# Kernel optimization log

Hardware: AMD Instinct MI355X
Metric: run time of the kernel (lower is better)

Reference implementation:

```python
import jax, jax.numpy as jnp
import numpy as np

NHEAD = 8


def setup_inputs() -> dict:
    key = jax.random.key(0)
    ks = jax.random.split(key, 11)
    B, N, T, D = 8, 64, 128, 512
    s = 1.0 / np.sqrt(D)
    x = jax.random.normal(ks[0], (B, N, T, D), dtype=jnp.float32)
    mask = jax.random.randint(ks[1], (B, N, T, 1), 0, 2).astype(jnp.float32)
    Wq = jax.random.normal(ks[2], (D, D), dtype=jnp.float32) * s
    bq = jax.random.normal(ks[3], (D,), dtype=jnp.float32) * 0.01
    Wk = jax.random.normal(ks[4], (D, D), dtype=jnp.float32) * s
    bk = jax.random.normal(ks[5], (D,), dtype=jnp.float32) * 0.01
    Wv = jax.random.normal(ks[6], (D, D), dtype=jnp.float32) * s
    bv = jax.random.normal(ks[7], (D,), dtype=jnp.float32) * 0.01
    Wo = jax.random.normal(ks[8], (D, D), dtype=jnp.float32) * s
    bo = jax.random.normal(ks[9], (D,), dtype=jnp.float32) * 0.01
    return {"x": x, "mask": mask, "Wq": Wq, "bq": bq, "Wk": Wk, "bk": bk,
            "Wv": Wv, "bv": bv, "Wo": Wo, "bo": bo}


def _attention(x, mask, Wq, bq, Wk, bk, Wv, bv, Wo, bo):
    B, N, T, D = x.shape
    H = NHEAD
    Dh = D // H
    xf = x.reshape(B * N, T, D)  # fold batch*num_node
    # QKV projections -> [BN, H, T, Dh]
    Q = (xf @ Wq + bq).reshape(B * N, T, H, Dh).transpose(0, 2, 1, 3)
    K = (xf @ Wk + bk).reshape(B * N, T, H, Dh).transpose(0, 2, 1, 3)
    V = (xf @ Wv + bv).reshape(B * N, T, H, Dh).transpose(0, 2, 1, 3)
    # outer-product mask: [BN, 1, T, T], broadcasts over heads
    mf = mask.reshape(B * N, T)
    cmask = (mf[:, :, None] * mf[:, None, :])[:, None, :, :]
    valid = cmask != 0
    scale = 1.0 / jnp.sqrt(jnp.float32(Dh))
    scores = jnp.einsum('bhqd,bhkd->bhqk', Q, K) * scale  # [BN,H,T,T]
    # masked softmax; fully-masked rows become 0 (matches softmax -> nan_to_num)
    s = jnp.where(valid, scores, -1e30)
    m = jnp.max(s, axis=-1, keepdims=True)
    e = jnp.where(valid, jnp.exp(s - m), 0.0)
    denom = jnp.sum(e, axis=-1, keepdims=True)
    attn = jnp.where(denom > 0, e / jnp.where(denom > 0, denom, 1.0), 0.0)
    out = jnp.einsum('bhqk,bhkd->bhqd', attn, V)  # [BN,H,T,Dh]
    out = out.transpose(0, 2, 1, 3).reshape(B * N, T, D)
    out = out @ Wo + bo
    return out.reshape(B, N, T, D)


def reference(x, mask, Wq, bq, Wk, bk, Wv, bv, Wo, bo):
    return _attention(x, mask, Wq, bq, Wk, bk, Wv, bv, Wo, bo)
```

## Files before the change

kernel.cpp:

```cpp
#include <hip/hip_runtime.h>
#include <hip/hip_bf16.h>

#define BN   512
#define TT   128
#define DD   512
#define HH   8
#define DH   64
#define MTOT (BN * TT)

typedef __attribute__((ext_vector_type(8))) _Float16 half8v;
typedef __attribute__((ext_vector_type(4))) float    float4v;

#define AS1 __attribute__((address_space(1)))
#define AS3 __attribute__((address_space(3)))

union Hbits { _Float16 f; ushort u; };

__global__ __launch_bounds__(256)
void cvt_x(const float* __restrict__ X, _Float16* __restrict__ Xh) {
    const size_t total = (size_t)MTOT * DD / 4;
    for (size_t i = (size_t)blockIdx.x * 256 + threadIdx.x; i < total;
         i += (size_t)gridDim.x * 256) {
        float4 v = *(const float4*)(X + i * 4);
        Hbits h0, h1, h2, h3;
        h0.f = (_Float16)v.x; h1.f = (_Float16)v.y;
        h2.f = (_Float16)v.z; h3.f = (_Float16)v.w;
        *(ushort4*)(Xh + i * 4) = make_ushort4(h0.u, h1.u, h2.u, h3.u);
    }
}

__global__ __launch_bounds__(256)
void cvt_w(const float* __restrict__ W, _Float16* __restrict__ Wh) {
    int idx = blockIdx.x * 256 + threadIdx.x;
    int n = idx >> 9;
    int k = idx & 511;
    Wh[(size_t)n * DD + k] = (_Float16)W[(size_t)k * DD + n];
}

template <int MODE>
__global__ __launch_bounds__(256)
void gemm_mfma(const _Float16* __restrict__ A,
               const _Float16* __restrict__ W0,
               const _Float16* __restrict__ W1,
               const _Float16* __restrict__ W2,
               const float* __restrict__ b0, const float* __restrict__ b1,
               const float* __restrict__ b2,
               void* __restrict__ O0, void* __restrict__ O1,
               void* __restrict__ O2) {
    __shared__ _Float16 Alds[128 * 64];
    __shared__ _Float16 Blds[128 * 64];

    const int mt = blockIdx.x, nt = blockIdx.y, wz = blockIdx.z;
    const _Float16* Bt = (wz == 0) ? W0 : (wz == 1) ? W1 : W2;
    const float* bias = (wz == 0) ? b0 : (wz == 1) ? b1 : b2;

    const int tid = threadIdx.x;
    const int lane = tid & 63;
    const int wid = tid >> 6;
    const int wr = wid >> 1, wc = wid & 1;
    const int m0 = mt * 128, n0 = nt * 128;

    float4v acc[4][4] = {};

    for (int kt = 0; kt < 8; ++kt) {
        const int k0 = kt * 64;
        __syncthreads();
#pragma unroll
        for (int r = 0; r < 4; ++r) {
            const int ubase = r * 256 + wid * 64;
            const int u = ubase + lane;
            const int row = u >> 3, c = u & 7;
            const int csrc = c ^ (row & 7);
            const _Float16* gpA = A + (size_t)(m0 + row) * DD + k0 + csrc * 8;
            __builtin_amdgcn_global_load_lds(
                (const AS1 void*)gpA, (AS3 void*)(Alds + ubase * 8), 16, 0, 0);
            const _Float16* gpB = Bt + (size_t)(n0 + row) * DD + k0 + csrc * 8;
            __builtin_amdgcn_global_load_lds(
                (const AS1 void*)gpB, (AS3 void*)(Blds + ubase * 8), 16, 0, 0);
        }
        __syncthreads();

#pragma unroll
        for (int ks = 0; ks < 2; ++ks) {
            const int g = ks * 4 + (lane >> 4);
            const int cswz = (g ^ (lane & 7)) * 8;
            half8v a[4], b[4];
#pragma unroll
            for (int i = 0; i < 4; ++i)
                a[i] = *(const half8v*)(Alds +
                        (size_t)(wr * 64 + i * 16 + (lane & 15)) * 64 + cswz);
#pragma unroll
            for (int j = 0; j < 4; ++j)
                b[j] = *(const half8v*)(Blds +
                        (size_t)(wc * 64 + j * 16 + (lane & 15)) * 64 + cswz);
#pragma unroll
            for (int i = 0; i < 4; ++i)
#pragma unroll
                for (int j = 0; j < 4; ++j)
                    acc[i][j] = __builtin_amdgcn_mfma_f32_16x16x32_f16(
                        a[i], b[j], acc[i][j], 0, 0, 0);
        }
    }

    const int cr = (lane >> 4) * 4;
    const int cc0 = lane & 15;
    if (MODE == 0) {
        float* C = (float*)((wz == 0) ? O0 : (wz == 1) ? O1 : O2);
#pragma unroll
        for (int j = 0; j < 4; ++j) {
            const int col = n0 + wc * 64 + j * 16 + cc0;
            const float bv = bias[col];
#pragma unroll
            for (int i = 0; i < 4; ++i) {
                const size_t rbase = (size_t)(m0 + wr * 64 + i * 16 + cr);
#pragma unroll
                for (int rg = 0; rg < 4; ++rg)
                    C[(rbase + rg) * DD + col] = acc[i][j][rg] + bv;
            }
        }
    } else if (wz < 2) {
        _Float16* C = (_Float16*)((wz == 0) ? O0 : O1);
#pragma unroll
        for (int j = 0; j < 4; ++j) {
            const int col = n0 + wc * 64 + j * 16 + cc0;
            const float bv = bias[col];
#pragma unroll
            for (int i = 0; i < 4; ++i) {
                const size_t rbase = (size_t)(m0 + wr * 64 + i * 16 + cr);
#pragma unroll
                for (int rg = 0; rg < 4; ++rg)
                    C[(rbase + rg) * DD + col] = (_Float16)(acc[i][j][rg] + bv);
            }
        }
    } else {
        _Float16* Vt = (_Float16*)O2;
        const int bnq = m0 >> 7;
#pragma unroll
        for (int j = 0; j < 4; ++j) {
            const int col = n0 + wc * 64 + j * 16 + cc0;
            const int hh = col >> 6, d = col & 63;
            const float bv = bias[col];
#pragma unroll
            for (int i = 0; i < 4; ++i) {
                const int t0 = wr * 64 + i * 16 + cr;
                Hbits e0, e1, e2, e3;
                e0.f = (_Float16)(acc[i][j][0] + bv);
                e1.f = (_Float16)(acc[i][j][1] + bv);
                e2.f = (_Float16)(acc[i][j][2] + bv);
                e3.f = (_Float16)(acc[i][j][3] + bv);
                *(ushort4*)(Vt + ((size_t)(bnq * 8 + hh) * 64 + d) * 128 + t0)
                    = make_ushort4(e0.u, e1.u, e2.u, e3.u);
            }
        }
    }
}

__global__ __launch_bounds__(256)
void attn_mfma(const _Float16* __restrict__ Qh, const _Float16* __restrict__ Kh,
               const _Float16* __restrict__ Vt, const float* __restrict__ mask,
               _Float16* __restrict__ Oh) {
    __shared__ _Float16 KP[128 * 128];
    __shared__ _Float16 Vl[64 * 128];
    __shared__ float maskS[TT];

    const int bnh = blockIdx.x, bn = bnh >> 3, h = bnh & 7;
    const int tid = threadIdx.x, lane = tid & 63, wid = tid >> 6;
    const int l15 = lane & 15, l16 = lane >> 4;

    if (tid < TT) maskS[tid] = mask[bn * TT + tid];

#pragma unroll
    for (int it = 0; it < 4; ++it) {
        const int ubase = it * 256 + wid * 64;
        const int u = ubase + lane;
        const int row = u >> 3, c = u & 7;
        const _Float16* gp = Kh + (size_t)(bn * TT + row) * DD + h * DH +
                             (c ^ (row & 7)) * 8;
        __builtin_amdgcn_global_load_lds(
            (const AS1 void*)gp, (AS3 void*)(KP + ubase * 8), 16, 0, 0);
    }
#pragma unroll
    for (int it = 0; it < 4; ++it) {
        const int ubase = it * 256 + wid * 64;
        const int u = ubase + lane;
        const int row = u >> 4, c = u & 15;
        const _Float16* gp = Vt + ((size_t)(bn * HH + h) * 64 + row) * 128 +
                             (c ^ (row & 15)) * 8;
        __builtin_amdgcn_global_load_lds(
            (const AS1 void*)gp, (AS3 void*)(Vl + ubase * 8), 16, 0, 0);
    }
    half8v qf[2][2];
#pragma unroll
    for (int i = 0; i < 2; ++i)
#pragma unroll
        for (int ks = 0; ks < 2; ++ks)
            qf[i][ks] = *(const half8v*)(Qh +
                (size_t)(bn * TT + wid * 32 + i * 16 + l15) * DD +
                h * DH + ks * 32 + l16 * 8);
    __syncthreads();

    float4v s[2][8] = {};
#pragma unroll
    for (int ks = 0; ks < 2; ++ks) {
#pragma unroll
        for (int j = 0; j < 8; ++j) {
            const int row = j * 16 + l15;
            const int g = ks * 4 + l16;
            half8v bf = *(const half8v*)(KP + (size_t)row * 64 +
                                         ((g ^ (l15 & 7)) * 8));
            s[0][j] = __builtin_amdgcn_mfma_f32_16x16x32_f16(
                qf[0][ks], bf, s[0][j], 0, 0, 0);
            s[1][j] = __builtin_amdgcn_mfma_f32_16x16x32_f16(
                qf[1][ks], bf, s[1][j], 0, 0, 0);
        }
    }

    float lrow[2][4];
#pragma unroll
    for (int i = 0; i < 2; ++i) {
#pragma unroll
        for (int reg = 0; reg < 4; ++reg) {
            const int q = wid * 32 + i * 16 + l16 * 4 + reg;
            const float rv = maskS[q];
            float mx = -1e30f;
#pragma unroll
            for (int j = 0; j < 8; ++j) {
                const bool valid = (rv != 0.f) && (maskS[j * 16 + l15] != 0.f);
                const float sv = valid ? s[i][j][reg] * 0.125f : -1e30f;
                s[i][j][reg] = sv;
                mx = fmaxf(mx, sv);
            }
#pragma unroll
            for (int d = 1; d < 16; d <<= 1) mx = fmaxf(mx, __shfl_xor(mx, d));
            float ls = 0.f;
#pragma unroll
            for (int j = 0; j < 8; ++j) {
                const float sv = s[i][j][reg];
                const float pv = (sv > -1e29f) ? __expf(sv - mx) : 0.f;
                s[i][j][reg] = pv;
                ls += pv;
            }
#pragma unroll
            for (int d = 1; d < 16; d <<= 1) ls += __shfl_xor(ls, d);
            lrow[i][reg] = ls;
        }
    }

    __syncthreads();
#pragma unroll
    for (int i = 0; i < 2; ++i)
#pragma unroll
        for (int j = 0; j < 8; ++j)
#pragma unroll
            for (int reg = 0; reg < 4; ++reg) {
                const int q = wid * 32 + i * 16 + l16 * 4 + reg;
                const int kv = j * 16 + l15;
                const int c = kv >> 3, o = kv & 7;
                KP[(size_t)q * 128 + ((c ^ (q & 15)) * 8 + o)] =
                    (_Float16)s[i][j][reg];
            }
    __syncthreads();

    float4v o_[2][4] = {};
#pragma unroll
    for (int ks = 0; ks < 4; ++ks) {
        half8v a[2];
#pragma unroll
        for (int i = 0; i < 2; ++i) {
            const int row = wid * 32 + i * 16 + l15;
            const int g = ks * 4 + l16;
            a[i] = *(const half8v*)(KP + (size_t)row * 128 + ((g ^ l15) * 8));
        }
#pragma unroll
        for (int j = 0; j < 4; ++j) {
            const int row = j * 16 + l15;
            const int g = ks * 4 + l16;
            half8v bv = *(const half8v*)(Vl + (size_t)row * 128 +
                                         ((g ^ l15) * 8));
#pragma unroll
            for (int i = 0; i < 2; ++i)
                o_[i][j] = __builtin_amdgcn_mfma_f32_16x16x32_f16(
                    a[i], bv, o_[i][j], 0, 0, 0);
        }
    }

#pragma unroll
    for (int i = 0; i < 2; ++i)
#pragma unroll
        for (int reg = 0; reg < 4; ++reg) {
            const float l = lrow[i][reg];
            const float inv = (l > 0.f) ? 1.f / l : 0.f;
            const size_t grow = (size_t)bn * TT + wid * 32 + i * 16 +
                                l16 * 4 + reg;
#pragma unroll
            for (int j = 0; j < 4; ++j) {
                const int d = j * 16 + l15;
                Oh[grow * DD + h * DH + d] = (_Float16)(o_[i][j][reg] * inv);
            }
        }
}

extern "C" void kernel_launch(void* const* d_in, const int* in_sizes, int n_in,
                              void* d_out, int out_size, void* d_ws, size_t ws_size,
                              hipStream_t stream) {
    const float* x    = (const float*)d_in[0];
    const float* mask = (const float*)d_in[1];
    const float* Wq   = (const float*)d_in[2];
    const float* bq   = (const float*)d_in[3];
    const float* Wk   = (const float*)d_in[4];
    const float* bk   = (const float*)d_in[5];
    const float* Wv   = (const float*)d_in[6];
    const float* bv   = (const float*)d_in[7];
    const float* Wo   = (const float*)d_in[8];
    const float* bo   = (const float*)d_in[9];
    float* out = (float*)d_out;

    const size_t elems = (size_t)MTOT * DD;
    _Float16* Xh  = (_Float16*)d_ws;
    _Float16* Qh  = Xh + elems;
    _Float16* Kh  = Qh + elems;
    _Float16* Vtb = Kh + elems;
    _Float16* Oh  = Vtb + elems;
    _Float16* Wh  = Oh + elems;

    cvt_x<<<2048, 256, 0, stream>>>(x, Xh);
    cvt_w<<<1024, 256, 0, stream>>>(Wq, Wh + 0 * (size_t)DD * DD);
    cvt_w<<<1024, 256, 0, stream>>>(Wk, Wh + 1 * (size_t)DD * DD);
    cvt_w<<<1024, 256, 0, stream>>>(Wv, Wh + 2 * (size_t)DD * DD);
    cvt_w<<<1024, 256, 0, stream>>>(Wo, Wh + 3 * (size_t)DD * DD);

    gemm_mfma<1><<<dim3(512, 4, 3), 256, 0, stream>>>(
        Xh, Wh + 0 * (size_t)DD * DD, Wh + 1 * (size_t)DD * DD,
        Wh + 2 * (size_t)DD * DD, bq, bk, bv, Qh, Kh, Vtb);
    attn_mfma<<<dim3(BN * HH), 256, 0, stream>>>(Qh, Kh, Vtb, mask, Oh);
    gemm_mfma<0><<<dim3(512, 4, 1), 256, 0, stream>>>(
        Oh, Wh + 3 * (size_t)DD * DD, nullptr, nullptr, bo, bo, bo,
        out, out, out);
}
```

Measured before the change: 601.9 us.

## Double-buffer GEMM LDS tiles, remap grid for A-tile reuse, merge weight conversions

Switches the GEMM main loop to two LDS buffers so the next K-tile's global-to-LDS load is issued before the MFMAs on the current tile, with one barrier per iteration instead of two. The grid is flattened and reordered so consecutive blocks share the same M tile across all N tiles and weight matrices, which improves L2 reuse of the activation rows. The four weight-conversion launches are merged into one launch. LDS use doubles to 64KB per block, which may lower occupancy.

```diff
diff --git a/kernel.cpp b/kernel.cpp
--- a/kernel.cpp
+++ b/kernel.cpp
@@ -30,11 +30,16 @@
 }
 
 __global__ __launch_bounds__(256)
-void cvt_w(const float* __restrict__ W, _Float16* __restrict__ Wh) {
+void cvt_w4(const float* __restrict__ W0, const float* __restrict__ W1,
+            const float* __restrict__ W2, const float* __restrict__ W3,
+            _Float16* __restrict__ Wh) {
+    const int z = blockIdx.y;
+    const float* W = (z == 0) ? W0 : (z == 1) ? W1 : (z == 2) ? W2 : W3;
+    _Float16* dst = Wh + (size_t)z * DD * DD;
     int idx = blockIdx.x * 256 + threadIdx.x;
     int n = idx >> 9;
     int k = idx & 511;
-    Wh[(size_t)n * DD + k] = (_Float16)W[(size_t)k * DD + n];
+    dst[(size_t)n * DD + k] = (_Float16)W[(size_t)k * DD + n];
 }
 
 template <int MODE>
@@ -47,10 +52,21 @@
                const float* __restrict__ b2,
                void* __restrict__ O0, void* __restrict__ O1,
                void* __restrict__ O2) {
-    __shared__ _Float16 Alds[128 * 64];
-    __shared__ _Float16 Blds[128 * 64];
-
-    const int mt = blockIdx.x, nt = blockIdx.y, wz = blockIdx.z;
+    __shared__ _Float16 Alds[2][128 * 64];
+    __shared__ _Float16 Blds[2][128 * 64];
+
+    const int bid = blockIdx.x;
+    int mt, nt, wz;
+    if (MODE == 1) {
+        mt = bid / 12;
+        const int r = bid - mt * 12;
+        wz = r >> 2;
+        nt = r & 3;
+    } else {
+        mt = bid >> 2;
+        nt = bid & 3;
+        wz = 0;
+    }
     const _Float16* Bt = (wz == 0) ? W0 : (wz == 1) ? W1 : W2;
     const float* bias = (wz == 0) ? b0 : (wz == 1) ? b1 : b2;
 
@@ -60,26 +76,32 @@
     const int wr = wid >> 1, wc = wid & 1;
     const int m0 = mt * 128, n0 = nt * 128;
 
-    float4v acc[4][4] = {};
-
-    for (int kt = 0; kt < 8; ++kt) {
-        const int k0 = kt * 64;
-        __syncthreads();
+    auto STAGE = [&](int kt, int buf) {
 #pragma unroll
         for (int r = 0; r < 4; ++r) {
             const int ubase = r * 256 + wid * 64;
             const int u = ubase + lane;
             const int row = u >> 3, c = u & 7;
             const int csrc = c ^ (row & 7);
-            const _Float16* gpA = A + (size_t)(m0 + row) * DD + k0 + csrc * 8;
+            const _Float16* gpA = A + (size_t)(m0 + row) * DD + kt * 64 + csrc * 8;
             __builtin_amdgcn_global_load_lds(
-                (const AS1 void*)gpA, (AS3 void*)(Alds + ubase * 8), 16, 0, 0);
-            const _Float16* gpB = Bt + (size_t)(n0 + row) * DD + k0 + csrc * 8;
+                (const AS1 void*)gpA, (AS3 void*)(&Alds[buf][ubase * 8]),
+                16, 0, 0);
+            const _Float16* gpB = Bt + (size_t)(n0 + row) * DD + kt * 64 + csrc * 8;
             __builtin_amdgcn_global_load_lds(
-                (const AS1 void*)gpB, (AS3 void*)(Blds + ubase * 8), 16, 0, 0);
-        }
-        __syncthreads();
-
+                (const AS1 void*)gpB, (AS3 void*)(&Blds[buf][ubase * 8]),
+                16, 0, 0);
+        }
+    };
+
+    float4v acc[4][4] = {};
+
+    STAGE(0, 0);
+    __syncthreads();
+
+    int cur = 0;
+    for (int kt = 0; kt < 8; ++kt) {
+        if (kt < 7) STAGE(kt + 1, cur ^ 1);
 #pragma unroll
         for (int ks = 0; ks < 2; ++ks) {
             const int g = ks * 4 + (lane >> 4);
@@ -87,12 +109,12 @@
             half8v a[4], b[4];
 #pragma unroll
             for (int i = 0; i < 4; ++i)
-                a[i] = *(const half8v*)(Alds +
-                        (size_t)(wr * 64 + i * 16 + (lane & 15)) * 64 + cswz);
+                a[i] = *(const half8v*)(&Alds[cur][
+                        (size_t)(wr * 64 + i * 16 + (lane & 15)) * 64 + cswz]);
 #pragma unroll
             for (int j = 0; j < 4; ++j)
-                b[j] = *(const half8v*)(Blds +
-                        (size_t)(wc * 64 + j * 16 + (lane & 15)) * 64 + cswz);
+                b[j] = *(const half8v*)(&Blds[cur][
+                        (size_t)(wc * 64 + j * 16 + (lane & 15)) * 64 + cswz]);
 #pragma unroll
             for (int i = 0; i < 4; ++i)
 #pragma unroll
@@ -100,6 +122,8 @@
                     acc[i][j] = __builtin_amdgcn_mfma_f32_16x16x32_f16(
                         a[i], b[j], acc[i][j], 0, 0, 0);
         }
+        __syncthreads();
+        cur ^= 1;
     }
 
     const int cr = (lane >> 4) * 4;
@@ -324,16 +348,13 @@
     _Float16* Wh  = Oh + elems;
 
     cvt_x<<<2048, 256, 0, stream>>>(x, Xh);
-    cvt_w<<<1024, 256, 0, stream>>>(Wq, Wh + 0 * (size_t)DD * DD);
-    cvt_w<<<1024, 256, 0, stream>>>(Wk, Wh + 1 * (size_t)DD * DD);
-    cvt_w<<<1024, 256, 0, stream>>>(Wv, Wh + 2 * (size_t)DD * DD);
-    cvt_w<<<1024, 256, 0, stream>>>(Wo, Wh + 3 * (size_t)DD * DD);
-
-    gemm_mfma<1><<<dim3(512, 4, 3), 256, 0, stream>>>(
+    cvt_w4<<<dim3(1024, 4), 256, 0, stream>>>(Wq, Wk, Wv, Wo, Wh);
+
+    gemm_mfma<1><<<512 * 12, 256, 0, stream>>>(
         Xh, Wh + 0 * (size_t)DD * DD, Wh + 1 * (size_t)DD * DD,
         Wh + 2 * (size_t)DD * DD, bq, bk, bv, Qh, Kh, Vtb);
     attn_mfma<<<dim3(BN * HH), 256, 0, stream>>>(Qh, Kh, Vtb, mask, Oh);
-    gemm_mfma<0><<<dim3(512, 4, 1), 256, 0, stream>>>(
+    gemm_mfma<0><<<512 * 4, 256, 0, stream>>>(
         Oh, Wh + 3 * (size_t)DD * DD, nullptr, nullptr, bo, bo, bo,
         out, out, out);
 }
```

Result: faster. 577.7 us (-4.0%).
